# Optimization experiments

Hardware: AMD Instinct MI355X
Metric: run time of the kernel (lower is better)

## Reference

```python
import jax, jax.numpy as jnp
import numpy as np

N = 262144          # nodes (512x512 GoL grid)
E = 2097152         # directed edges (8 neighbors per cell)
HID = 200           # MLP hidden width
DIMS = [1] + [HID] * 7 + [1]   # MLP(1, 200, 1, num_layers=8)


def setup_inputs() -> dict:
    key = jax.random.key(0)
    ks = jax.random.split(key, 2 + 2 * 8)
    inp = {
        "x": jax.random.normal(ks[0], (N, 1), dtype=jnp.float32),
        "edge_index": jax.random.randint(ks[1], (2, E), 0, N, dtype=jnp.int64),
    }
    for i in range(8):
        fan_in = DIMS[i]
        bound = 1.0 / np.sqrt(fan_in)
        inp[f"W{i}"] = jax.random.uniform(ks[2 + 2 * i], (DIMS[i], DIMS[i + 1]),
                                          minval=-bound, maxval=bound, dtype=jnp.float32)
        inp[f"b{i}"] = jax.random.uniform(ks[3 + 2 * i], (DIMS[i + 1],),
                                          minval=-bound, maxval=bound, dtype=jnp.float32)
    return inp


def gcn_aggregate(x, edge_index):
    # Parameter-free GCNConv: add self-loops, symmetric deg normalization, scatter-add.
    src, dst = edge_index[0], edge_index[1]
    loop = jnp.arange(N, dtype=edge_index.dtype)
    s = jnp.concatenate([src, loop])
    d = jnp.concatenate([dst, loop])
    deg = jax.ops.segment_sum(jnp.ones((s.shape[0],), dtype=x.dtype), d, num_segments=N)
    inv_sqrt = jax.lax.rsqrt(jnp.maximum(deg, 1.0))        # deg >= 1 with self-loops
    norm = (inv_sqrt[s] * inv_sqrt[d])[:, None]            # [E+N, 1]
    msg = x[s] * norm                                      # gather + scale
    return jax.ops.segment_sum(msg, d, num_segments=N)     # scatter-add [N, 1]


def reference(x, edge_index, W0, b0, W1, b1, W2, b2, W3, b3, W4, b4, W5, b5, W6, b6, W7, b7):
    h = gcn_aggregate(x, edge_index)
    Ws = [W0, W1, W2, W3, W4, W5, W6, W7]
    bs = [b0, b1, b2, b3, b4, b5, b6, b7]
    for i in range(8):
        h = h @ Ws[i] + bs[i]
        if i < 7:
            h = jax.nn.relu(h)
    return jax.nn.sigmoid(h)   # [N, 1]
```

## Files before the change

### kernel.cpp

```cpp
#include <hip/hip_runtime.h>
#include <math.h>

#define N_NODES 262144
#define N_EDGES 2097152
#define NB 512
#define CAP 5120
#define NAH 256
#define EPB (N_EDGES / NAH)
#define HID 200
#define G_TAB 128
#define RLO (-8.0f)
#define RHI (8.0f)

__global__ __launch_bounds__(1024, 4)
void kA(const int4* __restrict__ src4, const int4* __restrict__ dst4,
        unsigned* __restrict__ gcur, unsigned* __restrict__ elist,
        const float* __restrict__ W0, const float* __restrict__ B0,
        const float* __restrict__ W1, const float* __restrict__ B1,
        const float* __restrict__ W2, const float* __restrict__ B2,
        const float* __restrict__ W3, const float* __restrict__ B3,
        const float* __restrict__ W4, const float* __restrict__ B4,
        const float* __restrict__ W5, const float* __restrict__ B5,
        const float* __restrict__ W6, const float* __restrict__ B6,
        const float* __restrict__ W7, const float* __restrict__ B7,
        float* __restrict__ T) {
    __shared__ float smf[2 * 256 + 4 * 256 + 8];
    unsigned* smu = (unsigned*)smf;
    const int tid = threadIdx.x;
    const int b = blockIdx.x;

    if (b < NAH) {
        unsigned* h = smu;
        unsigned* cur = smu + 512;
        if (tid < NB) h[tid] = 0u;
        __syncthreads();
        int base0 = b * (EPB / 4);
        #pragma unroll
        for (int i = 0; i < EPB / 4096; i++) {
            int4 d = dst4[base0 + i * 1024 + tid];
            atomicAdd(&h[d.x >> 9], 1u);
            atomicAdd(&h[d.y >> 9], 1u);
            atomicAdd(&h[d.z >> 9], 1u);
            atomicAdd(&h[d.w >> 9], 1u);
        }
        __syncthreads();
        if (tid < NB)
            cur[tid] = tid * CAP + atomicAdd(&gcur[tid], h[tid]);
        __syncthreads();
        #pragma unroll
        for (int i = 0; i < EPB / 4096; i++) {
            int4 sv = src4[base0 + i * 1024 + tid];
            int4 dv = dst4[base0 + i * 1024 + tid];
            unsigned p;
            p = atomicAdd(&cur[dv.x >> 9], 1u);
            elist[p] = ((unsigned)sv.x << 9) | (unsigned)(dv.x & 511);
            p = atomicAdd(&cur[dv.y >> 9], 1u);
            elist[p] = ((unsigned)sv.y << 9) | (unsigned)(dv.y & 511);
            p = atomicAdd(&cur[dv.z >> 9], 1u);
            elist[p] = ((unsigned)sv.z << 9) | (unsigned)(dv.z & 511);
            p = atomicAdd(&cur[dv.w >> 9], 1u);
            elist[p] = ((unsigned)sv.w << 9) | (unsigned)(dv.w & 511);
        }
    } else {
        const int p = b - NAH;
        const int g = tid >> 8;
        const int n = tid & 255;
        float* hs = smf;
        float* ps = smf + 512;
        float step = (RHI - RLO) / (float)(G_TAB - 1);
        float gp = RLO + (float)p * step;

        if (g == 0 && n < HID) hs[n] = fmaxf(fmaf(gp, W0[n], B0[n]), 0.f);
        __syncthreads();

        const float* Ws[6] = {W1, W2, W3, W4, W5, W6};
        const float* Bs[6] = {B1, B2, B3, B4, B5, B6};
        int cur = 0;
        for (int l = 0; l < 6; l++) {
            float part = 0.f;
            if (n < HID) {
                const float* Wp = Ws[l] + (g * 50) * HID + n;
                const float* hp = hs + cur * 256 + g * 50;
                #pragma unroll
                for (int k = 0; k < 50; k++)
                    part = fmaf(hp[k], Wp[k * HID], part);
            }
            ps[g * 256 + n] = part;
            __syncthreads();
            if (g == 0 && n < HID) {
                float acc = ps[n] + ps[256 + n] + ps[512 + n] + ps[768 + n] + Bs[l][n];
                hs[(1 - cur) * 256 + n] = fmaxf(acc, 0.f);
            }
            __syncthreads();
            cur = 1 - cur;
        }
        if (g == 0) {
            float part = (n < HID) ? hs[cur * 256 + n] * W7[n] : 0.f;
            #pragma unroll
            for (int o = 32; o > 0; o >>= 1) part += __shfl_down(part, o);
            float* w4 = smf + 512 + 1024;
            if ((n & 63) == 0) w4[n >> 6] = part;
        }
        __syncthreads();
        if (tid == 0) T[p] = smf[512 + 1024] + smf[512 + 1025] +
                             smf[512 + 1026] + smf[512 + 1027] + B7[0];
    }
}

__global__ __launch_bounds__(512)
void kB(const unsigned* __restrict__ gcur, const unsigned* __restrict__ elist,
        const float* __restrict__ x, float* __restrict__ inv, float* __restrict__ y) {
    __shared__ unsigned cnt[NB];
    int t = threadIdx.x, b = blockIdx.x;
    cnt[t] = 0u;
    __syncthreads();
    unsigned lo = b * CAP, hi = b * CAP + gcur[b];
    for (unsigned j = lo + t; j < hi; j += 512)
        atomicAdd(&cnt[elist[j] & 511u], 1u);
    __syncthreads();
    int i = b * 512 + t;
    float iv = rsqrtf((float)(cnt[t] + 1u));
    inv[i] = iv;
    y[i] = x[i] * iv;
}

__global__ __launch_bounds__(512)
void kC(const unsigned* __restrict__ gcur, const unsigned* __restrict__ elist,
        const float* __restrict__ inv, const float* __restrict__ y,
        const float* __restrict__ T, float* __restrict__ out) {
    __shared__ float accf[NB];
    int t = threadIdx.x, b = blockIdx.x;
    accf[t] = 0.f;
    __syncthreads();
    unsigned lo = b * CAP, hi = b * CAP + gcur[b];
    for (unsigned j = lo + t; j < hi; j += 512) {
        unsigned p = elist[j];
        atomicAdd(&accf[p & 511u], y[p >> 9]);
    }
    __syncthreads();
    float inv_step = (float)(G_TAB - 1) / (RHI - RLO);
    int i = b * 512 + t;
    float g = inv[i] * (accf[t] + y[i]);
    float u = (g - RLO) * inv_step;
    int j = min(max((int)u, 0), G_TAB - 2);
    float fr = u - (float)j;
    float logit = fmaf(fr, T[j + 1] - T[j], T[j]);
    out[i] = 1.f / (1.f + expf(-logit));
}

extern "C" void kernel_launch(void* const* d_in, const int* in_sizes, int n_in,
                              void* d_out, int out_size, void* d_ws, size_t ws_size,
                              hipStream_t stream) {
    const float* x = (const float*)d_in[0];
    const int* e = (const int*)d_in[1];
    const int* src = e;
    const int* dst = e + N_EDGES;
    const float* W0 = (const float*)d_in[2];  const float* B0 = (const float*)d_in[3];
    const float* W1 = (const float*)d_in[4];  const float* B1 = (const float*)d_in[5];
    const float* W2 = (const float*)d_in[6];  const float* B2 = (const float*)d_in[7];
    const float* W3 = (const float*)d_in[8];  const float* B3 = (const float*)d_in[9];
    const float* W4 = (const float*)d_in[10]; const float* B4 = (const float*)d_in[11];
    const float* W5 = (const float*)d_in[12]; const float* B5 = (const float*)d_in[13];
    const float* W6 = (const float*)d_in[14]; const float* B6 = (const float*)d_in[15];
    const float* W7 = (const float*)d_in[16]; const float* B7 = (const float*)d_in[17];
    float* out = (float*)d_out;

    unsigned* wsu = (unsigned*)d_ws;
    unsigned* elist = wsu;
    unsigned* gcur  = elist + NB * CAP;
    float* inv = (float*)(gcur + NB);
    float* y   = inv + N_NODES;
    float* T   = y + N_NODES;

    hipMemsetAsync(gcur, 0, NB * sizeof(unsigned), stream);
    kA<<<NAH + G_TAB, 1024, 0, stream>>>(
        (const int4*)src, (const int4*)dst, gcur, elist,
        W0, B0, W1, B1, W2, B2, W3, B3, W4, B4, W5, B5, W6, B6, W7, B7, T);
    kB<<<NB, 512, 0, stream>>>(gcur, elist, x, inv, y);
    kC<<<NB, 512, 0, stream>>>(gcur, elist, inv, y, T, out);
}
```

Baseline: 147.8 us.

## Bucket edges locally in LDS per block instead of global atomic reservation

Each partition block now histograms its edges by destination bucket, prefix-scans the histogram in shared memory, scatters the edges into an LDS-sorted buffer, and writes that buffer out contiguously, along with a per-block offset table. This removes the global atomic cursor, the memset and the scattered global writes. kB and kC then read each bucket as 256 small segments, one per source block, with two threads per segment. The trade-offs are a serial-ish 9-step scan with many barriers, much larger shared memory per block (about 40KB), and short, uneven segment reads that may give poor coalescing and load balance in the consumer kernels.

```diff
diff --git a/kernel.cpp b/kernel.cpp
--- a/kernel.cpp
+++ b/kernel.cpp
@@ -4,17 +4,17 @@
 #define N_NODES 262144
 #define N_EDGES 2097152
 #define NB 512
-#define CAP 5120
 #define NAH 256
 #define EPB (N_EDGES / NAH)
+#define ROW 513
 #define HID 200
 #define G_TAB 128
 #define RLO (-8.0f)
 #define RHI (8.0f)
 
-__global__ __launch_bounds__(1024, 4)
+__global__ __launch_bounds__(1024)
 void kA(const int4* __restrict__ src4, const int4* __restrict__ dst4,
-        unsigned* __restrict__ gcur, unsigned* __restrict__ elist,
+        unsigned* __restrict__ elist, unsigned* __restrict__ bhoff,
         const float* __restrict__ W0, const float* __restrict__ B0,
         const float* __restrict__ W1, const float* __restrict__ B1,
         const float* __restrict__ W2, const float* __restrict__ B2,
@@ -24,44 +24,66 @@
         const float* __restrict__ W6, const float* __restrict__ B6,
         const float* __restrict__ W7, const float* __restrict__ B7,
         float* __restrict__ T) {
-    __shared__ float smf[2 * 256 + 4 * 256 + 8];
-    unsigned* smu = (unsigned*)smf;
+    __shared__ unsigned smu[512 + 512 + EPB];
     const int tid = threadIdx.x;
     const int b = blockIdx.x;
 
     if (b < NAH) {
         unsigned* h = smu;
         unsigned* cur = smu + 512;
-        if (tid < NB) h[tid] = 0u;
+        unsigned* sorted = smu + 1024;
+        if (tid < 512) h[tid] = 0u;
         __syncthreads();
         int base0 = b * (EPB / 4);
-        #pragma unroll
-        for (int i = 0; i < EPB / 4096; i++) {
-            int4 d = dst4[base0 + i * 1024 + tid];
-            atomicAdd(&h[d.x >> 9], 1u);
-            atomicAdd(&h[d.y >> 9], 1u);
-            atomicAdd(&h[d.z >> 9], 1u);
-            atomicAdd(&h[d.w >> 9], 1u);
-        }
-        __syncthreads();
-        if (tid < NB)
-            cur[tid] = tid * CAP + atomicAdd(&gcur[tid], h[tid]);
-        __syncthreads();
-        #pragma unroll
-        for (int i = 0; i < EPB / 4096; i++) {
-            int4 sv = src4[base0 + i * 1024 + tid];
-            int4 dv = dst4[base0 + i * 1024 + tid];
+        int4 dv[2], sv[2];
+        #pragma unroll
+        for (int i = 0; i < 2; i++) {
+            dv[i] = dst4[base0 + i * 1024 + tid];
+            sv[i] = src4[base0 + i * 1024 + tid];
+        }
+        #pragma unroll
+        for (int i = 0; i < 2; i++) {
+            atomicAdd(&h[dv[i].x >> 9], 1u);
+            atomicAdd(&h[dv[i].y >> 9], 1u);
+            atomicAdd(&h[dv[i].z >> 9], 1u);
+            atomicAdd(&h[dv[i].w >> 9], 1u);
+        }
+        __syncthreads();
+        unsigned mine = (tid < 512) ? h[tid] : 0u;
+        for (int o = 1; o < 512; o <<= 1) {
+            unsigned v = 0u;
+            if (tid < 512 && tid >= o) v = h[tid - o];
+            __syncthreads();
+            if (tid < 512) h[tid] += v;
+            __syncthreads();
+        }
+        if (tid < 512) {
+            unsigned excl = h[tid] - mine;
+            cur[tid] = excl;
+            bhoff[b * ROW + tid] = excl;
+            if (tid == 0) bhoff[b * ROW + 512] = EPB;
+        }
+        __syncthreads();
+        #pragma unroll
+        for (int i = 0; i < 2; i++) {
             unsigned p;
-            p = atomicAdd(&cur[dv.x >> 9], 1u);
-            elist[p] = ((unsigned)sv.x << 9) | (unsigned)(dv.x & 511);
-            p = atomicAdd(&cur[dv.y >> 9], 1u);
-            elist[p] = ((unsigned)sv.y << 9) | (unsigned)(dv.y & 511);
-            p = atomicAdd(&cur[dv.z >> 9], 1u);
-            elist[p] = ((unsigned)sv.z << 9) | (unsigned)(dv.z & 511);
-            p = atomicAdd(&cur[dv.w >> 9], 1u);
-            elist[p] = ((unsigned)sv.w << 9) | (unsigned)(dv.w & 511);
-        }
+            p = atomicAdd(&cur[dv[i].x >> 9], 1u);
+            sorted[p] = ((unsigned)sv[i].x << 9) | (unsigned)(dv[i].x & 511);
+            p = atomicAdd(&cur[dv[i].y >> 9], 1u);
+            sorted[p] = ((unsigned)sv[i].y << 9) | (unsigned)(dv[i].y & 511);
+            p = atomicAdd(&cur[dv[i].z >> 9], 1u);
+            sorted[p] = ((unsigned)sv[i].z << 9) | (unsigned)(dv[i].z & 511);
+            p = atomicAdd(&cur[dv[i].w >> 9], 1u);
+            sorted[p] = ((unsigned)sv[i].w << 9) | (unsigned)(dv[i].w & 511);
+        }
+        __syncthreads();
+        uint4* el4 = (uint4*)(elist + b * EPB);
+        const uint4* so4 = (const uint4*)sorted;
+        #pragma unroll
+        for (int i = 0; i < 2; i++)
+            el4[i * 1024 + tid] = so4[i * 1024 + tid];
     } else {
+        float* smf = (float*)smu;
         const int p = b - NAH;
         const int g = tid >> 8;
         const int n = tid & 255;
@@ -108,38 +130,44 @@
 }
 
 __global__ __launch_bounds__(512)
-void kB(const unsigned* __restrict__ gcur, const unsigned* __restrict__ elist,
+void kB(const unsigned* __restrict__ bhoff, const unsigned* __restrict__ elist,
         const float* __restrict__ x, float* __restrict__ inv, float* __restrict__ y) {
-    __shared__ unsigned cnt[NB];
-    int t = threadIdx.x, b = blockIdx.x;
+    __shared__ unsigned cnt[512];
+    int t = threadIdx.x, k = blockIdx.x;
     cnt[t] = 0u;
     __syncthreads();
-    unsigned lo = b * CAP, hi = b * CAP + gcur[b];
-    for (unsigned j = lo + t; j < hi; j += 512)
-        atomicAdd(&cnt[elist[j] & 511u], 1u);
-    __syncthreads();
-    int i = b * 512 + t;
+    int f = t >> 1, half = t & 1;
+    unsigned off = bhoff[f * ROW + k];
+    unsigned end = bhoff[f * ROW + k + 1];
+    const unsigned* ep = elist + f * EPB;
+    for (unsigned j = off + half; j < end; j += 2)
+        atomicAdd(&cnt[ep[j] & 511u], 1u);
+    __syncthreads();
+    int i = k * 512 + t;
     float iv = rsqrtf((float)(cnt[t] + 1u));
     inv[i] = iv;
     y[i] = x[i] * iv;
 }
 
 __global__ __launch_bounds__(512)
-void kC(const unsigned* __restrict__ gcur, const unsigned* __restrict__ elist,
+void kC(const unsigned* __restrict__ bhoff, const unsigned* __restrict__ elist,
         const float* __restrict__ inv, const float* __restrict__ y,
         const float* __restrict__ T, float* __restrict__ out) {
-    __shared__ float accf[NB];
-    int t = threadIdx.x, b = blockIdx.x;
+    __shared__ float accf[512];
+    int t = threadIdx.x, k = blockIdx.x;
     accf[t] = 0.f;
     __syncthreads();
-    unsigned lo = b * CAP, hi = b * CAP + gcur[b];
-    for (unsigned j = lo + t; j < hi; j += 512) {
-        unsigned p = elist[j];
+    int f = t >> 1, half = t & 1;
+    unsigned off = bhoff[f * ROW + k];
+    unsigned end = bhoff[f * ROW + k + 1];
+    const unsigned* ep = elist + f * EPB;
+    for (unsigned j = off + half; j < end; j += 2) {
+        unsigned p = ep[j];
         atomicAdd(&accf[p & 511u], y[p >> 9]);
     }
     __syncthreads();
     float inv_step = (float)(G_TAB - 1) / (RHI - RLO);
-    int i = b * 512 + t;
+    int i = k * 512 + t;
     float g = inv[i] * (accf[t] + y[i]);
     float u = (g - RLO) * inv_step;
     int j = min(max((int)u, 0), G_TAB - 2);
@@ -167,15 +195,14 @@
 
     unsigned* wsu = (unsigned*)d_ws;
     unsigned* elist = wsu;
-    unsigned* gcur  = elist + NB * CAP;
-    float* inv = (float*)(gcur + NB);
+    unsigned* bhoff = elist + N_EDGES;
+    float* inv = (float*)(bhoff + NAH * ROW);
     float* y   = inv + N_NODES;
     float* T   = y + N_NODES;
 
-    hipMemsetAsync(gcur, 0, NB * sizeof(unsigned), stream);
     kA<<<NAH + G_TAB, 1024, 0, stream>>>(
-        (const int4*)src, (const int4*)dst, gcur, elist,
+        (const int4*)src, (const int4*)dst, elist, bhoff,
         W0, B0, W1, B1, W2, B2, W3, B3, W4, B4, W5, B5, W6, B6, W7, B7, T);
-    kB<<<NB, 512, 0, stream>>>(gcur, elist, x, inv, y);
-    kC<<<NB, 512, 0, stream>>>(gcur, elist, inv, y, T, out);
-}
+    kB<<<NB, 512, 0, stream>>>(bhoff, elist, x, inv, y);
+    kC<<<NB, 512, 0, stream>>>(bhoff, elist, inv, y, T, out);
+}
```

New measurement: 146.2 us. Within noise of the previous version (-1.0%).
